# Kernel tuning notes

Measured on AMD Instinct MI355X. Metric: run time of the kernel, lower is better.

The kernel has to match this reference:

```python
import jax, jax.numpy as jnp
import numpy as np

B, S, E, H = 4, 8192, 1024, 16
D = E // H  # head_dim = 64


def setup_inputs() -> dict:
    key = jax.random.key(0)
    ks = jax.random.split(key, 9)
    s = 0.02
    return {
        "x": jax.random.normal(ks[0], (B, S, E), dtype=jnp.float32),
        "Wq": jax.random.normal(ks[1], (D, E), dtype=jnp.float32) * s,
        "bq": jax.random.normal(ks[2], (D,), dtype=jnp.float32) * s,
        "Wk": jax.random.normal(ks[3], (D, E), dtype=jnp.float32) * s,
        "bk": jax.random.normal(ks[4], (D,), dtype=jnp.float32) * s,
        "Wv": jax.random.normal(ks[5], (D, E), dtype=jnp.float32) * s,
        "bv": jax.random.normal(ks[6], (D,), dtype=jnp.float32) * s,
        "Wo": jax.random.normal(ks[7], (E, E), dtype=jnp.float32) * s,
        "bo": jax.random.normal(ks[8], (E,), dtype=jnp.float32) * s,
    }


def reference(x, Wq, bq, Wk, bk, Wv, bv, Wo, bo):
    b, s, e = x.shape
    d = Wq.shape[0]          # head_dim (projections map embed_dim -> head_dim)
    h = e // d               # num_heads
    # torch Linear: y = x @ W.T + b ; projected shape [B, S, d]
    # view(B, -1, h, d) on [B, S, d] => effective seq S' = S // h (faithful to source)
    def split_heads(t):
        return t.reshape(b, -1, h, d).transpose(0, 2, 1, 3)  # [B, H, S', D]
    q = split_heads(x @ Wq.T + bq)
    k = split_heads(x @ Wk.T + bk)
    v = split_heads(x @ Wv.T + bv)
    scores = jnp.einsum('bhqd,bhkd->bhqk', q, k) / np.sqrt(d).astype(jnp.float32)
    attn = jax.nn.softmax(scores, axis=-1)  # dropout=0.0 => identity
    ctx = jnp.einsum('bhqk,bhkd->bhqd', attn, v)
    ctx = ctx.transpose(0, 2, 1, 3).reshape(b, -1, e)  # [B, S', E]
    return ctx @ Wo.T + bo
```

## Files before the change

kernel.cpp:

```cpp
#include <hip/hip_runtime.h>
#include <hip/hip_bf16.h>


typedef unsigned short u16;
typedef __attribute__((ext_vector_type(8))) short short8;
typedef __attribute__((ext_vector_type(4))) float f32x4;

#define VMWAIT(N) asm volatile("s_waitcnt vmcnt(" #N ")" ::: "memory")
#define MEMFENCE() asm volatile("" ::: "memory")
#define BAR() __builtin_amdgcn_s_barrier()

__device__ inline u16 f2bf(float f) {
    union { float f; unsigned u; } v; v.f = f;
    unsigned u = v.u;
    return (u16)((u + 0x7fffu + ((u >> 16) & 1u)) >> 16);
}
__device__ inline unsigned pack_bf2(float a, float b) {
    union { __hip_bfloat162 h; unsigned u; } v;
    v.h = __float22bfloat162_rn(float2{a, b});
    return v.u;
}
__device__ __forceinline__ void gld16(void* lds, const void* gptr) {
    __builtin_amdgcn_global_load_lds(
        (const __attribute__((address_space(1))) unsigned int*)gptr,
        (__attribute__((address_space(3))) unsigned int*)lds,
        16, 0, 0);
}

__global__ __launch_bounds__(256) void convw(
    const float* __restrict__ Wq, const float* __restrict__ bq,
    const float* __restrict__ Wk, const float* __restrict__ bk,
    const float* __restrict__ Wv, const float* __restrict__ bv,
    const float* __restrict__ Wo,
    u16* __restrict__ Wqkv, float* __restrict__ qkvb, u16* __restrict__ Wob)
{
    const int idx = blockIdx.x * 256 + threadIdx.x;
    Wob[idx] = f2bf(Wo[idx]);
    if (idx < 196608) {
        const int row = idx >> 10, k = idx & 1023;
        float v = (row < 64)  ? Wq[row * 1024 + k] * 0.125f
                : (row < 128) ? Wk[(row - 64) * 1024 + k]
                              : Wv[(row - 128) * 1024 + k];
        Wqkv[idx] = f2bf(v);
    }
    if (idx < 192) {
        qkvb[idx] = (idx < 64) ? bq[idx] * 0.125f
                  : (idx < 128) ? bk[idx - 64] : bv[idx - 128];
    }
}

__global__ __launch_bounds__(256) void qkv_gemm(
    const float* __restrict__ X, const u16* __restrict__ W,
    const float* __restrict__ bias, u16* __restrict__ Out)
{
    __shared__ short8 Bs[2][1536];

    const int tid = threadIdx.x;
    const int lane = tid & 63, wid = tid >> 6;
    const int q = lane >> 4, r = lane & 15;
    const int wm = wid >> 1, wn = wid & 1;
    const long m0 = (long)blockIdx.x * 64;

    const u16* wp[6];
    #pragma unroll
    for (int i = 0; i < 6; ++i) {
        const int p = wid * 6 + i, kk2 = p / 12, nt = p % 12;
        wp[i] = W + (long)(nt * 16 + r) * 1024 + kk2 * 32 + q * 8;
    }

    const float* px0 = X + (m0 + wm * 32 + r) * 1024 + q * 8;
    const float* px1 = px0 + 16 * 1024;

    f32x4 acc[2][6] = {};

    float4 a[2][4];
    a[0][0] = *(const float4*)(px0);
    a[0][1] = *(const float4*)(px0 + 4);
    a[0][2] = *(const float4*)(px0 + 32);
    a[0][3] = *(const float4*)(px0 + 36);
    a[1][0] = *(const float4*)(px1);
    a[1][1] = *(const float4*)(px1 + 4);
    a[1][2] = *(const float4*)(px1 + 32);
    a[1][3] = *(const float4*)(px1 + 36);
    MEMFENCE();
    #pragma unroll
    for (int i = 0; i < 6; ++i)
        gld16(&Bs[0][(wid * 6 + i) * 64], wp[i]);

    for (int k0 = 0; k0 < 1024; k0 += 64) {
        const int buf = (k0 >> 6) & 1;
        float4 an[2][4];
        if (k0 + 64 < 1024) {
            an[0][0] = *(const float4*)(px0 + k0 + 64);
            an[0][1] = *(const float4*)(px0 + k0 + 68);
            an[0][2] = *(const float4*)(px0 + k0 + 96);
            an[0][3] = *(const float4*)(px0 + k0 + 100);
            an[1][0] = *(const float4*)(px1 + k0 + 64);
            an[1][1] = *(const float4*)(px1 + k0 + 68);
            an[1][2] = *(const float4*)(px1 + k0 + 96);
            an[1][3] = *(const float4*)(px1 + k0 + 100);
            MEMFENCE();
            #pragma unroll
            for (int i = 0; i < 6; ++i)
                gld16(&Bs[buf ^ 1][(wid * 6 + i) * 64], wp[i] + k0 + 64);
            VMWAIT(14);
        } else {
            VMWAIT(0);
        }
        BAR();
        MEMFENCE();
        #pragma unroll
        for (int kk2 = 0; kk2 < 2; ++kk2) {
            union { short8 s; unsigned u[4]; } af0, af1;
            af0.u[0] = pack_bf2(a[0][kk2 * 2].x, a[0][kk2 * 2].y);
            af0.u[1] = pack_bf2(a[0][kk2 * 2].z, a[0][kk2 * 2].w);
            af0.u[2] = pack_bf2(a[0][kk2 * 2 + 1].x, a[0][kk2 * 2 + 1].y);
            af0.u[3] = pack_bf2(a[0][kk2 * 2 + 1].z, a[0][kk2 * 2 + 1].w);
            af1.u[0] = pack_bf2(a[1][kk2 * 2].x, a[1][kk2 * 2].y);
            af1.u[1] = pack_bf2(a[1][kk2 * 2].z, a[1][kk2 * 2].w);
            af1.u[2] = pack_bf2(a[1][kk2 * 2 + 1].x, a[1][kk2 * 2 + 1].y);
            af1.u[3] = pack_bf2(a[1][kk2 * 2 + 1].z, a[1][kk2 * 2 + 1].w);
            #pragma unroll
            for (int j = 0; j < 6; ++j) {
                const short8 bf = Bs[buf][(kk2 * 12 + wn * 6 + j) * 64 + lane];
                acc[0][j] = __builtin_amdgcn_mfma_f32_16x16x32_bf16(
                    af0.s, bf, acc[0][j], 0, 0, 0);
                acc[1][j] = __builtin_amdgcn_mfma_f32_16x16x32_bf16(
                    af1.s, bf, acc[1][j], 0, 0, 0);
            }
        }
        MEMFENCE();
        BAR();
        if (k0 + 64 < 1024) {
            #pragma unroll
            for (int mf = 0; mf < 2; ++mf)
                #pragma unroll
                for (int i = 0; i < 4; ++i) a[mf][i] = an[mf][i];
        }
    }

    u16* lds0 = (u16*)&Bs[0][0];
    #pragma unroll
    for (int j = 0; j < 6; ++j) {
        const int col = wn * 96 + j * 16 + r;
        const float badd = bias[col];
        #pragma unroll
        for (int mf = 0; mf < 2; ++mf)
            #pragma unroll
            for (int e = 0; e < 4; ++e)
                lds0[(wm * 32 + mf * 16 + q * 4 + e) * 192 + col] =
                    f2bf(acc[mf][j][e] + badd);
    }
    asm volatile("s_waitcnt lgkmcnt(0)" ::: "memory");
    BAR();
    const short8* l8 = (const short8*)lds0;
    u16* ob = Out + m0 * 192;
    #pragma unroll
    for (int s = 0; s < 6; ++s) {
        short8 v = l8[tid + s * 256];
        *(short8*)(ob + (long)(tid + s * 256) * 8) = v;
    }
}

__global__ __launch_bounds__(256) void vtrans(
    const u16* __restrict__ qkv, u16* __restrict__ Vt)
{
    __shared__ u16 T[64][68];
    const int bh = blockIdx.x, b = bh >> 4, h = bh & 15;
    const int i0 = blockIdx.y * 64;
    const int tid = threadIdx.x;

    #pragma unroll
    for (int it = 0; it < 2; ++it) {
        const int c = tid + 256 * it;
        const int il = c >> 3, d8 = (c & 7) * 8;
        short8 v = *(const short8*)(qkv +
            ((long)b * 8192 + (long)(i0 + il) * 16 + h) * 192 + 128 + d8);
        #pragma unroll
        for (int j = 0; j < 8; ++j) T[d8 + j][il] = (u16)v[j];
    }
    __syncthreads();
    #pragma unroll
    for (int it = 0; it < 2; ++it) {
        const int c = tid + 256 * it;
        const int dl = c >> 3, i8 = (c & 7) * 8;
        short8 o;
        #pragma unroll
        for (int j = 0; j < 8; ++j) o[j] = (short)T[dl][i8 + j];
        *(short8*)(Vt + ((long)bh * 64 + dl) * 512 + i0 + i8) = o;
    }
}

__global__ __launch_bounds__(256) void attn_flash(
    const u16* __restrict__ qkv, const u16* __restrict__ Vt,
    u16* __restrict__ ctx)
{
    __shared__ short8 Ks[2][512];
    __shared__ short8 Vs[2][512];
    __shared__ u16 Plds[4][16 * 72];

    const int tid = threadIdx.x, lane = tid & 63, wid = tid >> 6;
    const int q = lane >> 4, r = lane & 15;
    const int qt = blockIdx.x;
    const int bh = blockIdx.y;
    const int b = bh >> 4, h = bh & 15;
    const long qrowbase = (long)b * 8192 + h;

    short8 Qf0, Qf1;
    {
        const int i = qt * 64 + wid * 16 + r;
        const u16* p = qkv + (qrowbase + (long)i * 16) * 192 + q * 8;
        Qf0 = *(const short8*)(p);
        Qf1 = *(const short8*)(p + 32);
    }

    const u16* kbase = qkv + (qrowbase + (long)(wid * 16 + r) * 16) * 192
                           + 64 + q * 8;
    const u16* vbase = Vt + ((long)bh * 64 + wid * 16 + r) * 512 + q * 8;

    gld16(&Ks[0][wid * 64],       kbase);
    gld16(&Ks[0][256 + wid * 64], kbase + 32);
    gld16(&Vs[0][wid * 64],       vbase);
    gld16(&Vs[0][256 + wid * 64], vbase + 32);

    f32x4 O[4] = {};
    float mrun = -1e30f, lrun = 0.f;
    u16* Pw = &Plds[wid][0];

    for (int c = 0; c < 8; ++c) {
        const int j0 = c * 64, buf = c & 1;
        if (c < 7) {
            const u16* kp = kbase + (long)(j0 + 64) * 3072;
            const u16* vp = vbase + j0 + 64;
            gld16(&Ks[buf ^ 1][wid * 64],       kp);
            gld16(&Ks[buf ^ 1][256 + wid * 64], kp + 32);
            gld16(&Vs[buf ^ 1][wid * 64],       vp);
            gld16(&Vs[buf ^ 1][256 + wid * 64], vp + 32);
            VMWAIT(4);
        } else {
            VMWAIT(0);
        }
        BAR();
        MEMFENCE();
        f32x4 S[4];
        #pragma unroll
        for (int ct = 0; ct < 4; ++ct) {
            f32x4 s = {};
            s = __builtin_amdgcn_mfma_f32_16x16x32_bf16(
                Ks[buf][ct * 64 + lane], Qf0, s, 0, 0, 0);
            s = __builtin_amdgcn_mfma_f32_16x16x32_bf16(
                Ks[buf][256 + ct * 64 + lane], Qf1, s, 0, 0, 0);
            S[ct] = s;
        }
        float mc = -1e30f;
        #pragma unroll
        for (int ct = 0; ct < 4; ++ct)
            mc = fmaxf(mc, fmaxf(fmaxf(S[ct][0], S[ct][1]),
                                 fmaxf(S[ct][2], S[ct][3])));
        mc = fmaxf(mc, __shfl_xor(mc, 16, 64));
        mc = fmaxf(mc, __shfl_xor(mc, 32, 64));
        const float mnew = fmaxf(mrun, mc);
        const float alpha = __expf(mrun - mnew);
        mrun = mnew;
        float se = 0.f;
        #pragma unroll
        for (int ct = 0; ct < 4; ++ct)
            #pragma unroll
            for (int e = 0; e < 4; ++e) {
                const float pv = __expf(S[ct][e] - mnew);
                S[ct][e] = pv; se += pv;
            }
        se += __shfl_xor(se, 16, 64);
        se += __shfl_xor(se, 32, 64);
        lrun = lrun * alpha + se;
        #pragma unroll
        for (int nt = 0; nt < 4; ++nt)
            #pragma unroll
            for (int e = 0; e < 4; ++e) O[nt][e] *= alpha;
        #pragma unroll
        for (int ct = 0; ct < 4; ++ct) {
            uint2 d;
            d.x = pack_bf2(S[ct][0], S[ct][1]);
            d.y = pack_bf2(S[ct][2], S[ct][3]);
            *(uint2*)(Pw + r * 72 + ct * 16 + q * 4) = d;
        }
        short8 Pf0 = *(const short8*)(Pw + r * 72 + q * 8);
        short8 Pf1 = *(const short8*)(Pw + r * 72 + 32 + q * 8);
        #pragma unroll
        for (int nt = 0; nt < 4; ++nt) {
            O[nt] = __builtin_amdgcn_mfma_f32_16x16x32_bf16(
                Vs[buf][nt * 64 + lane], Pf0, O[nt], 0, 0, 0);
            O[nt] = __builtin_amdgcn_mfma_f32_16x16x32_bf16(
                Vs[buf][256 + nt * 64 + lane], Pf1, O[nt], 0, 0, 0);
        }
        MEMFENCE();
        BAR();
    }

    const float inv = 1.0f / lrun;
    const long i = qt * 64 + wid * 16 + r;
    u16* po = ctx + ((long)b * 512 + i) * 1024 + h * 64;
    #pragma unroll
    for (int nt = 0; nt < 4; ++nt) {
        uint2 d;
        d.x = pack_bf2(O[nt][0] * inv, O[nt][1] * inv);
        d.y = pack_bf2(O[nt][2] * inv, O[nt][3] * inv);
        *(uint2*)(po + nt * 16 + q * 4) = d;
    }
}

__global__ __launch_bounds__(256) void gemm_o(
    const u16* __restrict__ A, const u16* __restrict__ B,
    const float* __restrict__ bias, float* __restrict__ C)
{
    __shared__ short8 As[2][512];
    __shared__ short8 Bs[2][512];

    const int tid = threadIdx.x;
    const int lane = tid & 63, wid = tid >> 6;
    const int q = lane >> 4, r = lane & 15;
    const long m0 = (long)blockIdx.x * 64, n0 = (long)blockIdx.y * 64;
    const int wm = wid >> 1, wn = wid & 1;

    const u16* ap[2];
    const u16* bp[2];
    #pragma unroll
    for (int i = 0; i < 2; ++i) {
        const int t = wid * 2 + i, f = t >> 2, mt = t & 3;
        ap[i] = A + (m0 + mt * 16 + r) * 1024 + f * 32 + q * 8;
        bp[i] = B + (n0 + mt * 16 + r) * 1024 + f * 32 + q * 8;
    }

    #pragma unroll
    for (int i = 0; i < 2; ++i) {
        gld16(&As[0][(wid * 2 + i) * 64], ap[i]);
        gld16(&Bs[0][(wid * 2 + i) * 64], bp[i]);
    }

    f32x4 acc[2][2] = {};

    for (int k0 = 0; k0 < 1024; k0 += 64) {
        const int buf = (k0 >> 6) & 1;
        if (k0 + 64 < 1024) {
            #pragma unroll
            for (int i = 0; i < 2; ++i) {
                gld16(&As[buf ^ 1][(wid * 2 + i) * 64], ap[i] + k0 + 64);
                gld16(&Bs[buf ^ 1][(wid * 2 + i) * 64], bp[i] + k0 + 64);
            }
            VMWAIT(4);
        } else {
            VMWAIT(0);
        }
        BAR();
        MEMFENCE();
        #pragma unroll
        for (int f = 0; f < 2; ++f) {
            short8 af0 = As[buf][f * 256 + (wm * 2 + 0) * 64 + lane];
            short8 af1 = As[buf][f * 256 + (wm * 2 + 1) * 64 + lane];
            short8 bf0 = Bs[buf][f * 256 + (wn * 2 + 0) * 64 + lane];
            short8 bf1 = Bs[buf][f * 256 + (wn * 2 + 1) * 64 + lane];
            acc[0][0] = __builtin_amdgcn_mfma_f32_16x16x32_bf16(af0, bf0, acc[0][0], 0, 0, 0);
            acc[0][1] = __builtin_amdgcn_mfma_f32_16x16x32_bf16(af0, bf1, acc[0][1], 0, 0, 0);
            acc[1][0] = __builtin_amdgcn_mfma_f32_16x16x32_bf16(af1, bf0, acc[1][0], 0, 0, 0);
            acc[1][1] = __builtin_amdgcn_mfma_f32_16x16x32_bf16(af1, bf1, acc[1][1], 0, 0, 0);
        }
        MEMFENCE();
        BAR();
    }

    #pragma unroll
    for (int i = 0; i < 2; ++i)
        #pragma unroll
        for (int j = 0; j < 2; ++j) {
            const long col = n0 + (wn * 2 + j) * 16 + r;
            const float badd = bias[col];
            #pragma unroll
            for (int e = 0; e < 4; ++e) {
                const long row = m0 + (wm * 2 + i) * 16 + q * 4 + e;
                C[row * 1024 + col] = acc[i][j][e] + badd;
            }
        }
}

extern "C" void kernel_launch(void* const* d_in, const int* in_sizes, int n_in,
                              void* d_out, int out_size, void* d_ws, size_t ws_size,
                              hipStream_t stream)
{
    const float* x  = (const float*)d_in[0];
    const float* Wq = (const float*)d_in[1];
    const float* bq = (const float*)d_in[2];
    const float* Wk = (const float*)d_in[3];
    const float* bk = (const float*)d_in[4];
    const float* Wv = (const float*)d_in[5];
    const float* bv = (const float*)d_in[6];
    const float* Wo = (const float*)d_in[7];
    const float* bo = (const float*)d_in[8];
    float* out = (float*)d_out;
    char* ws = (char*)d_ws;

    u16*   qkv  = (u16*)(ws);
    u16*   Vt   = (u16*)(ws + 12582912);
    u16*   Wqkv = (u16*)(ws + 16777216);
    u16*   Wob  = (u16*)(ws + 17170432);
    float* qkvb = (float*)(ws + 19267584);
    u16*   ctx  = (u16*)(ws + 19268352);

    convw<<<4096, 256, 0, stream>>>(Wq, bq, Wk, bk, Wv, bv, Wo, Wqkv, qkvb, Wob);
    qkv_gemm<<<512, 256, 0, stream>>>(x, Wqkv, qkvb, qkv);
    vtrans<<<dim3(64, 8), 256, 0, stream>>>(qkv, Vt);
    attn_flash<<<dim3(8, 64), 256, 0, stream>>>(qkv, Vt, ctx);
    gemm_o<<<dim3(32, 16), 256, 0, stream>>>(ctx, Wob, bo, out);
}
```

Before: 265.9 us.

## Deepen QKV GEMM pipeline to triple-buffered prefetch of X and W

```diff
diff --git a/kernel.cpp b/kernel.cpp
--- a/kernel.cpp
+++ b/kernel.cpp
@@ -49,11 +49,11 @@
     }
 }
 
-__global__ __launch_bounds__(256) void qkv_gemm(
+__global__ __launch_bounds__(256, 2) void qkv_gemm(
     const float* __restrict__ X, const u16* __restrict__ W,
     const float* __restrict__ bias, u16* __restrict__ Out)
 {
-    __shared__ short8 Bs[2][1536];
+    __shared__ short8 Bs[3][1536];
 
     const int tid = threadIdx.x;
     const int lane = tid & 63, wid = tid >> 6;
@@ -72,57 +72,54 @@
     const float* px1 = px0 + 16 * 1024;
 
     f32x4 acc[2][6] = {};
-
-    float4 a[2][4];
-    a[0][0] = *(const float4*)(px0);
-    a[0][1] = *(const float4*)(px0 + 4);
-    a[0][2] = *(const float4*)(px0 + 32);
-    a[0][3] = *(const float4*)(px0 + 36);
-    a[1][0] = *(const float4*)(px1);
-    a[1][1] = *(const float4*)(px1 + 4);
-    a[1][2] = *(const float4*)(px1 + 32);
-    a[1][3] = *(const float4*)(px1 + 36);
-    MEMFENCE();
-    #pragma unroll
-    for (int i = 0; i < 6; ++i)
-        gld16(&Bs[0][(wid * 6 + i) * 64], wp[i]);
-
-    for (int k0 = 0; k0 < 1024; k0 += 64) {
-        const int buf = (k0 >> 6) & 1;
-        float4 an[2][4];
-        if (k0 + 64 < 1024) {
-            an[0][0] = *(const float4*)(px0 + k0 + 64);
-            an[0][1] = *(const float4*)(px0 + k0 + 68);
-            an[0][2] = *(const float4*)(px0 + k0 + 96);
-            an[0][3] = *(const float4*)(px0 + k0 + 100);
-            an[1][0] = *(const float4*)(px1 + k0 + 64);
-            an[1][1] = *(const float4*)(px1 + k0 + 68);
-            an[1][2] = *(const float4*)(px1 + k0 + 96);
-            an[1][3] = *(const float4*)(px1 + k0 + 100);
-            MEMFENCE();
-            #pragma unroll
-            for (int i = 0; i < 6; ++i)
-                gld16(&Bs[buf ^ 1][(wid * 6 + i) * 64], wp[i] + k0 + 64);
-            VMWAIT(14);
-        } else {
-            VMWAIT(0);
-        }
+    float4 a[3][2][4];
+
+#define LOADA(s, j) do {                                            \
+        a[s][0][0] = *(const float4*)(px0 + (j) * 64);              \
+        a[s][0][1] = *(const float4*)(px0 + (j) * 64 + 4);          \
+        a[s][0][2] = *(const float4*)(px0 + (j) * 64 + 32);         \
+        a[s][0][3] = *(const float4*)(px0 + (j) * 64 + 36);         \
+        a[s][1][0] = *(const float4*)(px1 + (j) * 64);              \
+        a[s][1][1] = *(const float4*)(px1 + (j) * 64 + 4);          \
+        a[s][1][2] = *(const float4*)(px1 + (j) * 64 + 32);         \
+        a[s][1][3] = *(const float4*)(px1 + (j) * 64 + 36);         \
+    } while (0)
+
+#define STAGE(j) do {                                               \
+        _Pragma("unroll")                                           \
+        for (int i = 0; i < 6; ++i)                                 \
+            gld16(&Bs[(j) % 3][(wid * 6 + i) * 64], wp[i] + (j) * 64); \
+    } while (0)
+
+    LOADA(0, 0);  MEMFENCE();
+    STAGE(0);     MEMFENCE();
+    LOADA(1, 1);  MEMFENCE();
+    STAGE(1);     MEMFENCE();
+    LOADA(2, 2);  MEMFENCE();
+
+    #pragma unroll
+    for (int k = 0; k < 16; ++k) {
+        const int slot = k % 3;
+        if (k + 2 < 16) { STAGE(k + 2); MEMFENCE(); }
+        if (k < 14)      VMWAIT(28);
+        else if (k == 14) VMWAIT(14);
+        else             VMWAIT(0);
         BAR();
         MEMFENCE();
         #pragma unroll
         for (int kk2 = 0; kk2 < 2; ++kk2) {
             union { short8 s; unsigned u[4]; } af0, af1;
-            af0.u[0] = pack_bf2(a[0][kk2 * 2].x, a[0][kk2 * 2].y);
-            af0.u[1] = pack_bf2(a[0][kk2 * 2].z, a[0][kk2 * 2].w);
-            af0.u[2] = pack_bf2(a[0][kk2 * 2 + 1].x, a[0][kk2 * 2 + 1].y);
-            af0.u[3] = pack_bf2(a[0][kk2 * 2 + 1].z, a[0][kk2 * 2 + 1].w);
-            af1.u[0] = pack_bf2(a[1][kk2 * 2].x, a[1][kk2 * 2].y);
-            af1.u[1] = pack_bf2(a[1][kk2 * 2].z, a[1][kk2 * 2].w);
-            af1.u[2] = pack_bf2(a[1][kk2 * 2 + 1].x, a[1][kk2 * 2 + 1].y);
-            af1.u[3] = pack_bf2(a[1][kk2 * 2 + 1].z, a[1][kk2 * 2 + 1].w);
+            af0.u[0] = pack_bf2(a[slot][0][kk2 * 2].x, a[slot][0][kk2 * 2].y);
+            af0.u[1] = pack_bf2(a[slot][0][kk2 * 2].z, a[slot][0][kk2 * 2].w);
+            af0.u[2] = pack_bf2(a[slot][0][kk2 * 2 + 1].x, a[slot][0][kk2 * 2 + 1].y);
+            af0.u[3] = pack_bf2(a[slot][0][kk2 * 2 + 1].z, a[slot][0][kk2 * 2 + 1].w);
+            af1.u[0] = pack_bf2(a[slot][1][kk2 * 2].x, a[slot][1][kk2 * 2].y);
+            af1.u[1] = pack_bf2(a[slot][1][kk2 * 2].z, a[slot][1][kk2 * 2].w);
+            af1.u[2] = pack_bf2(a[slot][1][kk2 * 2 + 1].x, a[slot][1][kk2 * 2 + 1].y);
+            af1.u[3] = pack_bf2(a[slot][1][kk2 * 2 + 1].z, a[slot][1][kk2 * 2 + 1].w);
             #pragma unroll
             for (int j = 0; j < 6; ++j) {
-                const short8 bf = Bs[buf][(kk2 * 12 + wn * 6 + j) * 64 + lane];
+                const short8 bf = Bs[slot][(kk2 * 12 + wn * 6 + j) * 64 + lane];
                 acc[0][j] = __builtin_amdgcn_mfma_f32_16x16x32_bf16(
                     af0.s, bf, acc[0][j], 0, 0, 0);
                 acc[1][j] = __builtin_amdgcn_mfma_f32_16x16x32_bf16(
@@ -130,14 +127,11 @@
             }
         }
         MEMFENCE();
-        BAR();
-        if (k0 + 64 < 1024) {
-            #pragma unroll
-            for (int mf = 0; mf < 2; ++mf)
-                #pragma unroll
-                for (int i = 0; i < 4; ++i) a[mf][i] = an[mf][i];
-        }
-    }
+        if (k + 3 < 16) { LOADA(slot, k + 3); MEMFENCE(); }
+        BAR();
+    }
+#undef LOADA
+#undef STAGE
 
     u16* lds0 = (u16*)&Bs[0][0];
     #pragma unroll
```

After: 263.5 us. Within noise of the previous version (-0.9%).

## Fuse five kernels into one persistent kernel with grid-wide barriers

Applied to the files above, without the earlier changes.

```diff
diff --git a/kernel.cpp b/kernel.cpp
--- a/kernel.cpp
+++ b/kernel.cpp
@@ -27,359 +27,378 @@
         16, 0, 0);
 }
 
-__global__ __launch_bounds__(256) void convw(
+__device__ __forceinline__ void gbar(unsigned* cnt, unsigned* gen, unsigned nblk) {
+    __syncthreads();
+    if (threadIdx.x == 0) {
+        __threadfence();
+        unsigned g = __hip_atomic_load(gen, __ATOMIC_RELAXED,
+                                       __HIP_MEMORY_SCOPE_AGENT);
+        unsigned a = __hip_atomic_fetch_add(cnt, 1u, __ATOMIC_ACQ_REL,
+                                            __HIP_MEMORY_SCOPE_AGENT);
+        if (a + 1u == nblk) {
+            __hip_atomic_store(cnt, 0u, __ATOMIC_RELAXED,
+                               __HIP_MEMORY_SCOPE_AGENT);
+            __hip_atomic_store(gen, g + 1u, __ATOMIC_RELEASE,
+                               __HIP_MEMORY_SCOPE_AGENT);
+        } else {
+            while (__hip_atomic_load(gen, __ATOMIC_ACQUIRE,
+                                     __HIP_MEMORY_SCOPE_AGENT) == g)
+                __builtin_amdgcn_s_sleep(1);
+        }
+        __threadfence();
+    }
+    __syncthreads();
+}
+
+__global__ __launch_bounds__(256, 2) void mha_fused(
+    const float* __restrict__ X,
     const float* __restrict__ Wq, const float* __restrict__ bq,
     const float* __restrict__ Wk, const float* __restrict__ bk,
     const float* __restrict__ Wv, const float* __restrict__ bv,
-    const float* __restrict__ Wo,
-    u16* __restrict__ Wqkv, float* __restrict__ qkvb, u16* __restrict__ Wob)
+    const float* __restrict__ Wo, const float* __restrict__ bo,
+    float* __restrict__ out,
+    u16* __restrict__ qkv, u16* __restrict__ Vt, u16* __restrict__ Wqkv,
+    u16* __restrict__ Wob, float* __restrict__ qkvb, u16* __restrict__ ctx,
+    unsigned* __restrict__ bar)
 {
-    const int idx = blockIdx.x * 256 + threadIdx.x;
-    Wob[idx] = f2bf(Wo[idx]);
-    if (idx < 196608) {
-        const int row = idx >> 10, k = idx & 1023;
-        float v = (row < 64)  ? Wq[row * 1024 + k] * 0.125f
-                : (row < 128) ? Wk[(row - 64) * 1024 + k]
-                              : Wv[(row - 128) * 1024 + k];
-        Wqkv[idx] = f2bf(v);
-    }
-    if (idx < 192) {
-        qkvb[idx] = (idx < 64) ? bq[idx] * 0.125f
-                  : (idx < 128) ? bk[idx - 64] : bv[idx - 128];
-    }
-}
-
-__global__ __launch_bounds__(256) void qkv_gemm(
-    const float* __restrict__ X, const u16* __restrict__ W,
-    const float* __restrict__ bias, u16* __restrict__ Out)
-{
-    __shared__ short8 Bs[2][1536];
+    __shared__ __align__(16) char smraw[49152];
+
+    unsigned* bcnt = bar;
+    unsigned* bgen = bar + 1;
 
     const int tid = threadIdx.x;
+    const int bid = blockIdx.x;
     const int lane = tid & 63, wid = tid >> 6;
     const int q = lane >> 4, r = lane & 15;
-    const int wm = wid >> 1, wn = wid & 1;
-    const long m0 = (long)blockIdx.x * 64;
-
-    const u16* wp[6];
-    #pragma unroll
-    for (int i = 0; i < 6; ++i) {
-        const int p = wid * 6 + i, kk2 = p / 12, nt = p % 12;
-        wp[i] = W + (long)(nt * 16 + r) * 1024 + kk2 * 32 + q * 8;
-    }
-
-    const float* px0 = X + (m0 + wm * 32 + r) * 1024 + q * 8;
-    const float* px1 = px0 + 16 * 1024;
-
-    f32x4 acc[2][6] = {};
-
-    float4 a[2][4];
-    a[0][0] = *(const float4*)(px0);
-    a[0][1] = *(const float4*)(px0 + 4);
-    a[0][2] = *(const float4*)(px0 + 32);
-    a[0][3] = *(const float4*)(px0 + 36);
-    a[1][0] = *(const float4*)(px1);
-    a[1][1] = *(const float4*)(px1 + 4);
-    a[1][2] = *(const float4*)(px1 + 32);
-    a[1][3] = *(const float4*)(px1 + 36);
-    MEMFENCE();
-    #pragma unroll
-    for (int i = 0; i < 6; ++i)
-        gld16(&Bs[0][(wid * 6 + i) * 64], wp[i]);
-
-    for (int k0 = 0; k0 < 1024; k0 += 64) {
-        const int buf = (k0 >> 6) & 1;
-        float4 an[2][4];
-        if (k0 + 64 < 1024) {
-            an[0][0] = *(const float4*)(px0 + k0 + 64);
-            an[0][1] = *(const float4*)(px0 + k0 + 68);
-            an[0][2] = *(const float4*)(px0 + k0 + 96);
-            an[0][3] = *(const float4*)(px0 + k0 + 100);
-            an[1][0] = *(const float4*)(px1 + k0 + 64);
-            an[1][1] = *(const float4*)(px1 + k0 + 68);
-            an[1][2] = *(const float4*)(px1 + k0 + 96);
-            an[1][3] = *(const float4*)(px1 + k0 + 100);
-            MEMFENCE();
-            #pragma unroll
-            for (int i = 0; i < 6; ++i)
-                gld16(&Bs[buf ^ 1][(wid * 6 + i) * 64], wp[i] + k0 + 64);
-            VMWAIT(14);
-        } else {
-            VMWAIT(0);
-        }
+
+    for (int vb = bid; vb < 4096; vb += 512) {
+        const int idx = vb * 256 + tid;
+        Wob[idx] = f2bf(Wo[idx]);
+        if (idx < 196608) {
+            const int row = idx >> 10, k = idx & 1023;
+            float v = (row < 64)  ? Wq[row * 1024 + k] * 0.125f
+                    : (row < 128) ? Wk[(row - 64) * 1024 + k]
+                                  : Wv[(row - 128) * 1024 + k];
+            Wqkv[idx] = f2bf(v);
+        }
+        if (idx < 192) {
+            qkvb[idx] = (idx < 64) ? bq[idx] * 0.125f
+                      : (idx < 128) ? bk[idx - 64] : bv[idx - 128];
+        }
+    }
+    gbar(bcnt, bgen, 512);
+
+    {
+        short8 (*Bs)[1536] = reinterpret_cast<short8 (*)[1536]>(smraw);
+        const int wm = wid >> 1, wn = wid & 1;
+        const long m0 = (long)bid * 64;
+
+        const u16* wp[6];
+        #pragma unroll
+        for (int i = 0; i < 6; ++i) {
+            const int p = wid * 6 + i, kk2 = p / 12, nt = p % 12;
+            wp[i] = Wqkv + (long)(nt * 16 + r) * 1024 + kk2 * 32 + q * 8;
+        }
+        const float* px0 = X + (m0 + wm * 32 + r) * 1024 + q * 8;
+        const float* px1 = px0 + 16 * 1024;
+
+        f32x4 acc[2][6] = {};
+        float4 a[2][4];
+        a[0][0] = *(const float4*)(px0);
+        a[0][1] = *(const float4*)(px0 + 4);
+        a[0][2] = *(const float4*)(px0 + 32);
+        a[0][3] = *(const float4*)(px0 + 36);
+        a[1][0] = *(const float4*)(px1);
+        a[1][1] = *(const float4*)(px1 + 4);
+        a[1][2] = *(const float4*)(px1 + 32);
+        a[1][3] = *(const float4*)(px1 + 36);
+        MEMFENCE();
+        #pragma unroll
+        for (int i = 0; i < 6; ++i)
+            gld16(&Bs[0][(wid * 6 + i) * 64], wp[i]);
+
+        for (int k0 = 0; k0 < 1024; k0 += 64) {
+            const int buf = (k0 >> 6) & 1;
+            float4 an[2][4];
+            if (k0 + 64 < 1024) {
+                an[0][0] = *(const float4*)(px0 + k0 + 64);
+                an[0][1] = *(const float4*)(px0 + k0 + 68);
+                an[0][2] = *(const float4*)(px0 + k0 + 96);
+                an[0][3] = *(const float4*)(px0 + k0 + 100);
+                an[1][0] = *(const float4*)(px1 + k0 + 64);
+                an[1][1] = *(const float4*)(px1 + k0 + 68);
+                an[1][2] = *(const float4*)(px1 + k0 + 96);
+                an[1][3] = *(const float4*)(px1 + k0 + 100);
+                MEMFENCE();
+                #pragma unroll
+                for (int i = 0; i < 6; ++i)
+                    gld16(&Bs[buf ^ 1][(wid * 6 + i) * 64], wp[i] + k0 + 64);
+                VMWAIT(14);
+            } else {
+                VMWAIT(0);
+            }
+            BAR();
+            MEMFENCE();
+            #pragma unroll
+            for (int kk2 = 0; kk2 < 2; ++kk2) {
+                union { short8 s; unsigned u[4]; } af0, af1;
+                af0.u[0] = pack_bf2(a[0][kk2 * 2].x, a[0][kk2 * 2].y);
+                af0.u[1] = pack_bf2(a[0][kk2 * 2].z, a[0][kk2 * 2].w);
+                af0.u[2] = pack_bf2(a[0][kk2 * 2 + 1].x, a[0][kk2 * 2 + 1].y);
+                af0.u[3] = pack_bf2(a[0][kk2 * 2 + 1].z, a[0][kk2 * 2 + 1].w);
+                af1.u[0] = pack_bf2(a[1][kk2 * 2].x, a[1][kk2 * 2].y);
+                af1.u[1] = pack_bf2(a[1][kk2 * 2].z, a[1][kk2 * 2].w);
+                af1.u[2] = pack_bf2(a[1][kk2 * 2 + 1].x, a[1][kk2 * 2 + 1].y);
+                af1.u[3] = pack_bf2(a[1][kk2 * 2 + 1].z, a[1][kk2 * 2 + 1].w);
+                #pragma unroll
+                for (int j = 0; j < 6; ++j) {
+                    const short8 bf = Bs[buf][(kk2 * 12 + wn * 6 + j) * 64 + lane];
+                    acc[0][j] = __builtin_amdgcn_mfma_f32_16x16x32_bf16(
+                        af0.s, bf, acc[0][j], 0, 0, 0);
+                    acc[1][j] = __builtin_amdgcn_mfma_f32_16x16x32_bf16(
+                        af1.s, bf, acc[1][j], 0, 0, 0);
+                }
+            }
+            MEMFENCE();
+            BAR();
+            if (k0 + 64 < 1024) {
+                #pragma unroll
+                for (int mf = 0; mf < 2; ++mf)
+                    #pragma unroll
+                    for (int i = 0; i < 4; ++i) a[mf][i] = an[mf][i];
+            }
+        }
+
+        u16* lds0 = (u16*)&Bs[0][0];
+        #pragma unroll
+        for (int j = 0; j < 6; ++j) {
+            const int col = wn * 96 + j * 16 + r;
+            const float badd = qkvb[col];
+            #pragma unroll
+            for (int mf = 0; mf < 2; ++mf)
+                #pragma unroll
+                for (int e = 0; e < 4; ++e)
+                    lds0[(wm * 32 + mf * 16 + q * 4 + e) * 192 + col] =
+                        f2bf(acc[mf][j][e] + badd);
+        }
+        asm volatile("s_waitcnt lgkmcnt(0)" ::: "memory");
         BAR();
-        MEMFENCE();
-        #pragma unroll
-        for (int kk2 = 0; kk2 < 2; ++kk2) {
-            union { short8 s; unsigned u[4]; } af0, af1;
-            af0.u[0] = pack_bf2(a[0][kk2 * 2].x, a[0][kk2 * 2].y);
-            af0.u[1] = pack_bf2(a[0][kk2 * 2].z, a[0][kk2 * 2].w);
-            af0.u[2] = pack_bf2(a[0][kk2 * 2 + 1].x, a[0][kk2 * 2 + 1].y);
-            af0.u[3] = pack_bf2(a[0][kk2 * 2 + 1].z, a[0][kk2 * 2 + 1].w);
-            af1.u[0] = pack_bf2(a[1][kk2 * 2].x, a[1][kk2 * 2].y);
-            af1.u[1] = pack_bf2(a[1][kk2 * 2].z, a[1][kk2 * 2].w);
-            af1.u[2] = pack_bf2(a[1][kk2 * 2 + 1].x, a[1][kk2 * 2 + 1].y);
-            af1.u[3] = pack_bf2(a[1][kk2 * 2 + 1].z, a[1][kk2 * 2 + 1].w);
-            #pragma unroll
-            for (int j = 0; j < 6; ++j) {
-                const short8 bf = Bs[buf][(kk2 * 12 + wn * 6 + j) * 64 + lane];
-                acc[0][j] = __builtin_amdgcn_mfma_f32_16x16x32_bf16(
-                    af0.s, bf, acc[0][j], 0, 0, 0);
-                acc[1][j] = __builtin_amdgcn_mfma_f32_16x16x32_bf16(
-                    af1.s, bf, acc[1][j], 0, 0, 0);
-            }
-        }
-        MEMFENCE();
-        BAR();
-        if (k0 + 64 < 1024) {
-            #pragma unroll
-            for (int mf = 0; mf < 2; ++mf)
-                #pragma unroll
-                for (int i = 0; i < 4; ++i) a[mf][i] = an[mf][i];
-        }
-    }
-
-    u16* lds0 = (u16*)&Bs[0][0];
-    #pragma unroll
-    for (int j = 0; j < 6; ++j) {
-        const int col = wn * 96 + j * 16 + r;
-        const float badd = bias[col];
-        #pragma unroll
-        for (int mf = 0; mf < 2; ++mf)
-            #pragma unroll
-            for (int e = 0; e < 4; ++e)
-                lds0[(wm * 32 + mf * 16 + q * 4 + e) * 192 + col] =
-                    f2bf(acc[mf][j][e] + badd);
-    }
-    asm volatile("s_waitcnt lgkmcnt(0)" ::: "memory");
-    BAR();
-    const short8* l8 = (const short8*)lds0;
-    u16* ob = Out + m0 * 192;
-    #pragma unroll
-    for (int s = 0; s < 6; ++s) {
-        short8 v = l8[tid + s * 256];
-        *(short8*)(ob + (long)(tid + s * 256) * 8) = v;
-    }
-}
-
-__global__ __launch_bounds__(256) void vtrans(
-    const u16* __restrict__ qkv, u16* __restrict__ Vt)
-{
-    __shared__ u16 T[64][68];
-    const int bh = blockIdx.x, b = bh >> 4, h = bh & 15;
-    const int i0 = blockIdx.y * 64;
-    const int tid = threadIdx.x;
-
-    #pragma unroll
-    for (int it = 0; it < 2; ++it) {
-        const int c = tid + 256 * it;
-        const int il = c >> 3, d8 = (c & 7) * 8;
-        short8 v = *(const short8*)(qkv +
-            ((long)b * 8192 + (long)(i0 + il) * 16 + h) * 192 + 128 + d8);
-        #pragma unroll
-        for (int j = 0; j < 8; ++j) T[d8 + j][il] = (u16)v[j];
-    }
-    __syncthreads();
-    #pragma unroll
-    for (int it = 0; it < 2; ++it) {
-        const int c = tid + 256 * it;
-        const int dl = c >> 3, i8 = (c & 7) * 8;
-        short8 o;
-        #pragma unroll
-        for (int j = 0; j < 8; ++j) o[j] = (short)T[dl][i8 + j];
-        *(short8*)(Vt + ((long)bh * 64 + dl) * 512 + i0 + i8) = o;
-    }
-}
-
-__global__ __launch_bounds__(256) void attn_flash(
-    const u16* __restrict__ qkv, const u16* __restrict__ Vt,
-    u16* __restrict__ ctx)
-{
-    __shared__ short8 Ks[2][512];
-    __shared__ short8 Vs[2][512];
-    __shared__ u16 Plds[4][16 * 72];
-
-    const int tid = threadIdx.x, lane = tid & 63, wid = tid >> 6;
-    const int q = lane >> 4, r = lane & 15;
-    const int qt = blockIdx.x;
-    const int bh = blockIdx.y;
-    const int b = bh >> 4, h = bh & 15;
-    const long qrowbase = (long)b * 8192 + h;
-
-    short8 Qf0, Qf1;
+        const short8* l8 = (const short8*)lds0;
+        u16* ob = qkv + m0 * 192;
+        #pragma unroll
+        for (int s = 0; s < 6; ++s) {
+            short8 v = l8[tid + s * 256];
+            *(short8*)(ob + (long)(tid + s * 256) * 8) = v;
+        }
+    }
+    gbar(bcnt, bgen, 512);
+
     {
-        const int i = qt * 64 + wid * 16 + r;
-        const u16* p = qkv + (qrowbase + (long)i * 16) * 192 + q * 8;
-        Qf0 = *(const short8*)(p);
-        Qf1 = *(const short8*)(p + 32);
-    }
-
-    const u16* kbase = qkv + (qrowbase + (long)(wid * 16 + r) * 16) * 192
-                           + 64 + q * 8;
-    const u16* vbase = Vt + ((long)bh * 64 + wid * 16 + r) * 512 + q * 8;
-
-    gld16(&Ks[0][wid * 64],       kbase);
-    gld16(&Ks[0][256 + wid * 64], kbase + 32);
-    gld16(&Vs[0][wid * 64],       vbase);
-    gld16(&Vs[0][256 + wid * 64], vbase + 32);
-
-    f32x4 O[4] = {};
-    float mrun = -1e30f, lrun = 0.f;
-    u16* Pw = &Plds[wid][0];
-
-    for (int c = 0; c < 8; ++c) {
-        const int j0 = c * 64, buf = c & 1;
-        if (c < 7) {
-            const u16* kp = kbase + (long)(j0 + 64) * 3072;
-            const u16* vp = vbase + j0 + 64;
-            gld16(&Ks[buf ^ 1][wid * 64],       kp);
-            gld16(&Ks[buf ^ 1][256 + wid * 64], kp + 32);
-            gld16(&Vs[buf ^ 1][wid * 64],       vp);
-            gld16(&Vs[buf ^ 1][256 + wid * 64], vp + 32);
-            VMWAIT(4);
-        } else {
-            VMWAIT(0);
-        }
-        BAR();
-        MEMFENCE();
-        f32x4 S[4];
-        #pragma unroll
-        for (int ct = 0; ct < 4; ++ct) {
-            f32x4 s = {};
-            s = __builtin_amdgcn_mfma_f32_16x16x32_bf16(
-                Ks[buf][ct * 64 + lane], Qf0, s, 0, 0, 0);
-            s = __builtin_amdgcn_mfma_f32_16x16x32_bf16(
-                Ks[buf][256 + ct * 64 + lane], Qf1, s, 0, 0, 0);
-            S[ct] = s;
-        }
-        float mc = -1e30f;
-        #pragma unroll
-        for (int ct = 0; ct < 4; ++ct)
-            mc = fmaxf(mc, fmaxf(fmaxf(S[ct][0], S[ct][1]),
-                                 fmaxf(S[ct][2], S[ct][3])));
-        mc = fmaxf(mc, __shfl_xor(mc, 16, 64));
-        mc = fmaxf(mc, __shfl_xor(mc, 32, 64));
-        const float mnew = fmaxf(mrun, mc);
-        const float alpha = __expf(mrun - mnew);
-        mrun = mnew;
-        float se = 0.f;
-        #pragma unroll
-        for (int ct = 0; ct < 4; ++ct)
-            #pragma unroll
-            for (int e = 0; e < 4; ++e) {
-                const float pv = __expf(S[ct][e] - mnew);
-                S[ct][e] = pv; se += pv;
-            }
-        se += __shfl_xor(se, 16, 64);
-        se += __shfl_xor(se, 32, 64);
-        lrun = lrun * alpha + se;
-        #pragma unroll
-        for (int nt = 0; nt < 4; ++nt)
-            #pragma unroll
-            for (int e = 0; e < 4; ++e) O[nt][e] *= alpha;
-        #pragma unroll
-        for (int ct = 0; ct < 4; ++ct) {
+        u16 (*T)[68] = reinterpret_cast<u16 (*)[68]>(smraw);
+        const int bh = bid & 63, b = bh >> 4, h = bh & 15;
+        const int i0 = (bid >> 6) * 64;
+
+        #pragma unroll
+        for (int it = 0; it < 2; ++it) {
+            const int c = tid + 256 * it;
+            const int il = c >> 3, d8 = (c & 7) * 8;
+            short8 v = *(const short8*)(qkv +
+                ((long)b * 8192 + (long)(i0 + il) * 16 + h) * 192 + 128 + d8);
+            #pragma unroll
+            for (int j = 0; j < 8; ++j) T[d8 + j][il] = (u16)v[j];
+        }
+        __syncthreads();
+        #pragma unroll
+        for (int it = 0; it < 2; ++it) {
+            const int c = tid + 256 * it;
+            const int dl = c >> 3, i8 = (c & 7) * 8;
+            short8 o;
+            #pragma unroll
+            for (int j = 0; j < 8; ++j) o[j] = (short)T[dl][i8 + j];
+            *(short8*)(Vt + ((long)bh * 64 + dl) * 512 + i0 + i8) = o;
+        }
+    }
+    gbar(bcnt, bgen, 512);
+
+    {
+        short8 (*Ks)[512] = reinterpret_cast<short8 (*)[512]>(smraw);
+        short8 (*Vs)[512] = reinterpret_cast<short8 (*)[512]>(smraw + 16384);
+        u16* Plds = reinterpret_cast<u16*>(smraw + 32768);
+
+        const int qt = bid & 7, bh = bid >> 3;
+        const int b = bh >> 4, h = bh & 15;
+        const long qrowbase = (long)b * 8192 + h;
+
+        short8 Qf0, Qf1;
+        {
+            const int i = qt * 64 + wid * 16 + r;
+            const u16* p = qkv + (qrowbase + (long)i * 16) * 192 + q * 8;
+            Qf0 = *(const short8*)(p);
+            Qf1 = *(const short8*)(p + 32);
+        }
+
+        const u16* kbase = qkv + (qrowbase + (long)(wid * 16 + r) * 16) * 192
+                               + 64 + q * 8;
+        const u16* vbase = Vt + ((long)bh * 64 + wid * 16 + r) * 512 + q * 8;
+
+        gld16(&Ks[0][wid * 64],       kbase);
+        gld16(&Ks[0][256 + wid * 64], kbase + 32);
+        gld16(&Vs[0][wid * 64],       vbase);
+        gld16(&Vs[0][256 + wid * 64], vbase + 32);
+
+        f32x4 O[4] = {};
+        float mrun = -1e30f, lrun = 0.f;
+        u16* Pw = Plds + wid * 1152;
+
+        for (int c = 0; c < 8; ++c) {
+            const int j0 = c * 64, buf = c & 1;
+            if (c < 7) {
+                const u16* kp = kbase + (long)(j0 + 64) * 3072;
+                const u16* vp = vbase + j0 + 64;
+                gld16(&Ks[buf ^ 1][wid * 64],       kp);
+                gld16(&Ks[buf ^ 1][256 + wid * 64], kp + 32);
+                gld16(&Vs[buf ^ 1][wid * 64],       vp);
+                gld16(&Vs[buf ^ 1][256 + wid * 64], vp + 32);
+                VMWAIT(4);
+            } else {
+                VMWAIT(0);
+            }
+            BAR();
+            MEMFENCE();
+            f32x4 S[4];
+            #pragma unroll
+            for (int ct = 0; ct < 4; ++ct) {
+                f32x4 s = {};
+                s = __builtin_amdgcn_mfma_f32_16x16x32_bf16(
+                    Ks[buf][ct * 64 + lane], Qf0, s, 0, 0, 0);
+                s = __builtin_amdgcn_mfma_f32_16x16x32_bf16(
+                    Ks[buf][256 + ct * 64 + lane], Qf1, s, 0, 0, 0);
+                S[ct] = s;
+            }
+            float mc = -1e30f;
+            #pragma unroll
+            for (int ct = 0; ct < 4; ++ct)
+                mc = fmaxf(mc, fmaxf(fmaxf(S[ct][0], S[ct][1]),
+                                     fmaxf(S[ct][2], S[ct][3])));
+            mc = fmaxf(mc, __shfl_xor(mc, 16, 64));
+            mc = fmaxf(mc, __shfl_xor(mc, 32, 64));
+            const float mnew = fmaxf(mrun, mc);
+            const float alpha = __expf(mrun - mnew);
+            mrun = mnew;
+            float se = 0.f;
+            #pragma unroll
+            for (int ct = 0; ct < 4; ++ct)
+                #pragma unroll
+                for (int e = 0; e < 4; ++e) {
+                    const float pv = __expf(S[ct][e] - mnew);
+                    S[ct][e] = pv; se += pv;
+                }
+            se += __shfl_xor(se, 16, 64);
+            se += __shfl_xor(se, 32, 64);
+            lrun = lrun * alpha + se;
+            #pragma unroll
+            for (int nt = 0; nt < 4; ++nt)
+                #pragma unroll
+                for (int e = 0; e < 4; ++e) O[nt][e] *= alpha;
+            #pragma unroll
+            for (int ct = 0; ct < 4; ++ct) {
+                uint2 d;
+                d.x = pack_bf2(S[ct][0], S[ct][1]);
+                d.y = pack_bf2(S[ct][2], S[ct][3]);
+                *(uint2*)(Pw + r * 72 + ct * 16 + q * 4) = d;
+            }
+            short8 Pf0 = *(const short8*)(Pw + r * 72 + q * 8);
+            short8 Pf1 = *(const short8*)(Pw + r * 72 + 32 + q * 8);
+            #pragma unroll
+            for (int nt = 0; nt < 4; ++nt) {
+                O[nt] = __builtin_amdgcn_mfma_f32_16x16x32_bf16(
+                    Vs[buf][nt * 64 + lane], Pf0, O[nt], 0, 0, 0);
+                O[nt] = __builtin_amdgcn_mfma_f32_16x16x32_bf16(
+                    Vs[buf][256 + nt * 64 + lane], Pf1, O[nt], 0, 0, 0);
+            }
+            MEMFENCE();
+            BAR();
+        }
+
+        const float inv = 1.0f / lrun;
+        const long i = qt * 64 + wid * 16 + r;
+        u16* po = ctx + ((long)b * 512 + i) * 1024 + h * 64;
+        #pragma unroll
+        for (int nt = 0; nt < 4; ++nt) {
             uint2 d;
-            d.x = pack_bf2(S[ct][0], S[ct][1]);
-            d.y = pack_bf2(S[ct][2], S[ct][3]);
-            *(uint2*)(Pw + r * 72 + ct * 16 + q * 4) = d;
-        }
-        short8 Pf0 = *(const short8*)(Pw + r * 72 + q * 8);
-        short8 Pf1 = *(const short8*)(Pw + r * 72 + 32 + q * 8);
-        #pragma unroll
-        for (int nt = 0; nt < 4; ++nt) {
-            O[nt] = __builtin_amdgcn_mfma_f32_16x16x32_bf16(
-                Vs[buf][nt * 64 + lane], Pf0, O[nt], 0, 0, 0);
-            O[nt] = __builtin_amdgcn_mfma_f32_16x16x32_bf16(
-                Vs[buf][256 + nt * 64 + lane], Pf1, O[nt], 0, 0, 0);
-        }
-        MEMFENCE();
-        BAR();
-    }
-
-    const float inv = 1.0f / lrun;
-    const long i = qt * 64 + wid * 16 + r;
-    u16* po = ctx + ((long)b * 512 + i) * 1024 + h * 64;
-    #pragma unroll
-    for (int nt = 0; nt < 4; ++nt) {
-        uint2 d;
-        d.x = pack_bf2(O[nt][0] * inv, O[nt][1] * inv);
-        d.y = pack_bf2(O[nt][2] * inv, O[nt][3] * inv);
-        *(uint2*)(po + nt * 16 + q * 4) = d;
-    }
-}
-
-__global__ __launch_bounds__(256) void gemm_o(
-    const u16* __restrict__ A, const u16* __restrict__ B,
-    const float* __restrict__ bias, float* __restrict__ C)
-{
-    __shared__ short8 As[2][512];
-    __shared__ short8 Bs[2][512];
-
-    const int tid = threadIdx.x;
-    const int lane = tid & 63, wid = tid >> 6;
-    const int q = lane >> 4, r = lane & 15;
-    const long m0 = (long)blockIdx.x * 64, n0 = (long)blockIdx.y * 64;
-    const int wm = wid >> 1, wn = wid & 1;
-
-    const u16* ap[2];
-    const u16* bp[2];
-    #pragma unroll
-    for (int i = 0; i < 2; ++i) {
-        const int t = wid * 2 + i, f = t >> 2, mt = t & 3;
-        ap[i] = A + (m0 + mt * 16 + r) * 1024 + f * 32 + q * 8;
-        bp[i] = B + (n0 + mt * 16 + r) * 1024 + f * 32 + q * 8;
-    }
-
-    #pragma unroll
-    for (int i = 0; i < 2; ++i) {
-        gld16(&As[0][(wid * 2 + i) * 64], ap[i]);
-        gld16(&Bs[0][(wid * 2 + i) * 64], bp[i]);
-    }
-
-    f32x4 acc[2][2] = {};
-
-    for (int k0 = 0; k0 < 1024; k0 += 64) {
-        const int buf = (k0 >> 6) & 1;
-        if (k0 + 64 < 1024) {
-            #pragma unroll
-            for (int i = 0; i < 2; ++i) {
-                gld16(&As[buf ^ 1][(wid * 2 + i) * 64], ap[i] + k0 + 64);
-                gld16(&Bs[buf ^ 1][(wid * 2 + i) * 64], bp[i] + k0 + 64);
-            }
-            VMWAIT(4);
-        } else {
-            VMWAIT(0);
-        }
-        BAR();
-        MEMFENCE();
-        #pragma unroll
-        for (int f = 0; f < 2; ++f) {
-            short8 af0 = As[buf][f * 256 + (wm * 2 + 0) * 64 + lane];
-            short8 af1 = As[buf][f * 256 + (wm * 2 + 1) * 64 + lane];
-            short8 bf0 = Bs[buf][f * 256 + (wn * 2 + 0) * 64 + lane];
-            short8 bf1 = Bs[buf][f * 256 + (wn * 2 + 1) * 64 + lane];
-            acc[0][0] = __builtin_amdgcn_mfma_f32_16x16x32_bf16(af0, bf0, acc[0][0], 0, 0, 0);
-            acc[0][1] = __builtin_amdgcn_mfma_f32_16x16x32_bf16(af0, bf1, acc[0][1], 0, 0, 0);
-            acc[1][0] = __builtin_amdgcn_mfma_f32_16x16x32_bf16(af1, bf0, acc[1][0], 0, 0, 0);
-            acc[1][1] = __builtin_amdgcn_mfma_f32_16x16x32_bf16(af1, bf1, acc[1][1], 0, 0, 0);
-        }
-        MEMFENCE();
-        BAR();
-    }
-
-    #pragma unroll
-    for (int i = 0; i < 2; ++i)
-        #pragma unroll
-        for (int j = 0; j < 2; ++j) {
-            const long col = n0 + (wn * 2 + j) * 16 + r;
-            const float badd = bias[col];
-            #pragma unroll
-            for (int e = 0; e < 4; ++e) {
-                const long row = m0 + (wm * 2 + i) * 16 + q * 4 + e;
-                C[row * 1024 + col] = acc[i][j][e] + badd;
-            }
-        }
+            d.x = pack_bf2(O[nt][0] * inv, O[nt][1] * inv);
+            d.y = pack_bf2(O[nt][2] * inv, O[nt][3] * inv);
+            *(uint2*)(po + nt * 16 + q * 4) = d;
+        }
+    }
+    gbar(bcnt, bgen, 512);
+
+    {
+        short8 (*As)[512]  = reinterpret_cast<short8 (*)[512]>(smraw);
+        short8 (*Bs2)[512] = reinterpret_cast<short8 (*)[512]>(smraw + 16384);
+
+        const long m0 = (long)(bid & 31) * 64, n0 = (long)(bid >> 5) * 64;
+        const int wm = wid >> 1, wn = wid & 1;
+
+        const u16* ap[2];
+        const u16* bp[2];
+        #pragma unroll
+        for (int i = 0; i < 2; ++i) {
+            const int t = wid * 2 + i, f = t >> 2, mt = t & 3;
+            ap[i] = ctx + (m0 + mt * 16 + r) * 1024 + f * 32 + q * 8;
+            bp[i] = Wob + (n0 + mt * 16 + r) * 1024 + f * 32 + q * 8;
+        }
+
+        #pragma unroll
+        for (int i = 0; i < 2; ++i) {
+            gld16(&As[0][(wid * 2 + i) * 64], ap[i]);
+            gld16(&Bs2[0][(wid * 2 + i) * 64], bp[i]);
+        }
+
+        f32x4 acc[2][2] = {};
+
+        for (int k0 = 0; k0 < 1024; k0 += 64) {
+            const int buf = (k0 >> 6) & 1;
+            if (k0 + 64 < 1024) {
+                #pragma unroll
+                for (int i = 0; i < 2; ++i) {
+                    gld16(&As[buf ^ 1][(wid * 2 + i) * 64], ap[i] + k0 + 64);
+                    gld16(&Bs2[buf ^ 1][(wid * 2 + i) * 64], bp[i] + k0 + 64);
+                }
+                VMWAIT(4);
+            } else {
+                VMWAIT(0);
+            }
+            BAR();
+            MEMFENCE();
+            #pragma unroll
+            for (int f = 0; f < 2; ++f) {
+                short8 af0 = As[buf][f * 256 + (wm * 2 + 0) * 64 + lane];
+                short8 af1 = As[buf][f * 256 + (wm * 2 + 1) * 64 + lane];
+                short8 bf0 = Bs2[buf][f * 256 + (wn * 2 + 0) * 64 + lane];
+                short8 bf1 = Bs2[buf][f * 256 + (wn * 2 + 1) * 64 + lane];
+                acc[0][0] = __builtin_amdgcn_mfma_f32_16x16x32_bf16(af0, bf0, acc[0][0], 0, 0, 0);
+                acc[0][1] = __builtin_amdgcn_mfma_f32_16x16x32_bf16(af0, bf1, acc[0][1], 0, 0, 0);
+                acc[1][0] = __builtin_amdgcn_mfma_f32_16x16x32_bf16(af1, bf0, acc[1][0], 0, 0, 0);
+                acc[1][1] = __builtin_amdgcn_mfma_f32_16x16x32_bf16(af1, bf1, acc[1][1], 0, 0, 0);
+            }
+            MEMFENCE();
+            BAR();
+        }
+
+        #pragma unroll
+        for (int i = 0; i < 2; ++i)
+            #pragma unroll
+            for (int j = 0; j < 2; ++j) {
+                const long col = n0 + (wn * 2 + j) * 16 + r;
+                const float badd = bo[col];
+                #pragma unroll
+                for (int e = 0; e < 4; ++e) {
+                    const long row = m0 + (wm * 2 + i) * 16 + q * 4 + e;
+                    out[row * 1024 + col] = acc[i][j][e] + badd;
+                }
+            }
+    }
 }
 
 extern "C" void kernel_launch(void* const* d_in, const int* in_sizes, int n_in,
@@ -398,16 +417,17 @@
     float* out = (float*)d_out;
     char* ws = (char*)d_ws;
 
-    u16*   qkv  = (u16*)(ws);
-    u16*   Vt   = (u16*)(ws + 12582912);
-    u16*   Wqkv = (u16*)(ws + 16777216);
-    u16*   Wob  = (u16*)(ws + 17170432);
-    float* qkvb = (float*)(ws + 19267584);
-    u16*   ctx  = (u16*)(ws + 19268352);
-
-    convw<<<4096, 256, 0, stream>>>(Wq, bq, Wk, bk, Wv, bv, Wo, Wqkv, qkvb, Wob);
-    qkv_gemm<<<512, 256, 0, stream>>>(x, Wqkv, qkvb, qkv);
-    vtrans<<<dim3(64, 8), 256, 0, stream>>>(qkv, Vt);
-    attn_flash<<<dim3(8, 64), 256, 0, stream>>>(qkv, Vt, ctx);
-    gemm_o<<<dim3(32, 16), 256, 0, stream>>>(ctx, Wob, bo, out);
-}
+    u16*     qkv  = (u16*)(ws);
+    u16*     Vt   = (u16*)(ws + 12582912);
+    u16*     Wqkv = (u16*)(ws + 16777216);
+    u16*     Wob  = (u16*)(ws + 17170432);
+    float*   qkvb = (float*)(ws + 19267584);
+    u16*     ctx  = (u16*)(ws + 19268352);
+    unsigned* bar = (unsigned*)(ws + 25165824);
+
+    hipMemsetAsync(bar, 0, 16, stream);
+
+    mha_fused<<<512, 256, 0, stream>>>(
+        x, Wq, bq, Wk, bk, Wv, bv, Wo, bo, out,
+        qkv, Vt, Wqkv, Wob, qkvb, ctx, bar);
+}
```

Result: slower. 592.8 us (+122.9%).
